# Performance work log

Measured on AMD Instinct MI355X. Metric: run time of the kernel, lower is better.

Reference implementation:

```python
import jax, jax.numpy as jnp
import numpy as np

RHO = 1.0
EPSILON = 0.1
N_ITERS = 5
EPS = 1e-08


def setup_inputs() -> dict:
    key = jax.random.key(0)
    k1, k2, k3 = jax.random.split(key, 3)
    B, H, M, N, D = 16, 16, 256, 576, 1024
    # student cross-attention weights: positive, rows roughly sum to 1 (post-softmax in the real model)
    sa = jax.random.uniform(k1, (B, H, M, N), dtype=jnp.float32) + 1e-3
    student_attn = sa / sa.sum(axis=-1, keepdims=True)
    visual_feats = jax.random.normal(k2, (B, N, D), dtype=jnp.float32)
    text_feats = jax.random.normal(k3, (B, M, D), dtype=jnp.float32)
    text_mask = jnp.ones((B, M), dtype=jnp.float32)
    return {"student_attn": student_attn, "visual_feats": visual_feats,
            "text_feats": text_feats, "text_mask": text_mask}


def _l2norm(x):
    return x / jnp.sqrt(jnp.sum(x * x, axis=-1, keepdims=True) + 1e-12)


def _teacher_plan(x, y, y_mask):
    # x: (B,N,D) visual, y: (B,M,D) text, y_mask: (B,M)
    B, N, D = x.shape
    M = y.shape[1]
    x_n = _l2norm(x)
    y_n = _l2norm(y)
    cost = 1.0 - jnp.einsum('bmd,bnd->bmn', y_n, x_n)          # (B,M,N)
    mu = jnp.full((B, N, 1), 1.0 / N, dtype=x.dtype)            # visual marginal (column vec)
    nu = (y_mask / (jnp.sum(y_mask, axis=1, keepdims=True) + EPS))[:, :, None]  # (B,M,1)
    K = jnp.exp(-cost / EPSILON)                                # (B,M,N)
    fi = RHO / (RHO + EPSILON)
    u = jnp.ones((B, M, 1), dtype=x.dtype)
    v = jnp.ones((B, N, 1), dtype=x.dtype)
    for _ in range(N_ITERS):
        Kv = jnp.einsum('bmn,bnk->bmk', K, v)                   # (B,M,1)
        u = (nu / (Kv + EPS)) ** fi
        Ktu = jnp.einsum('bmn,bmk->bnk', K, u)                  # (B,N,1)
        v = (mu / (Ktu + EPS)) ** fi
    P = u * K * jnp.swapaxes(v, 1, 2)                           # (B,M,N)
    return P / (jnp.sum(P, axis=-1, keepdims=True) + EPS)


def reference(student_attn, visual_feats, text_feats, text_mask):
    teacher = jax.lax.stop_gradient(_teacher_plan(visual_feats, text_feats, text_mask))
    teacher = teacher[:, None, :, :]                            # (B,1,M,N)
    loss = -jnp.sum(teacher * jnp.log(student_attn + EPS), axis=-1)  # (B,H,M)
    loss = loss * text_mask[:, None, :]
    return jnp.mean(loss)
```

## Files before the change

### kernel.cpp

```cpp
#include <hip/hip_runtime.h>
#include <math.h>

#define B_ 16
#define H_ 16
#define M_ 256
#define N_ 576
#define D_ 1024
#define BK 64
#define LDS_STRIDE (BK + 8)

constexpr float EPS_ = 1e-8f;
constexpr float FI_ = 0.90909090909090906f;

typedef __bf16 bf16x8 __attribute__((ext_vector_type(8)));
typedef float f32x4 __attribute__((ext_vector_type(4)));

__device__ __forceinline__ float wave_reduce(float v) {
#pragma unroll
  for (int o = 32; o > 0; o >>= 1) v += __shfl_down(v, o, 64);
  return v;
}

__device__ __forceinline__ unsigned short f2bf(float f) {
  union { float f; unsigned u; } a; a.f = f;
  unsigned r = a.u + 0x7fff + ((a.u >> 16) & 1);
  return (unsigned short)(r >> 16);
}

__global__ __launch_bounds__(256) void norm_bf16_kernel(const float* __restrict__ x,
                                                        unsigned short* __restrict__ out,
                                                        int rows) {
  int wave = (int)((blockIdx.x * blockDim.x + threadIdx.x) >> 6);
  int lane = threadIdx.x & 63;
  if (wave >= rows) return;
  const float* r = x + (size_t)wave * D_;
  float4 v[4];
  float s = 0.f;
#pragma unroll
  for (int it = 0; it < 4; ++it) {
    v[it] = *(const float4*)&r[it * 256 + lane * 4];
    s += v[it].x * v[it].x + v[it].y * v[it].y + v[it].z * v[it].z + v[it].w * v[it].w;
  }
  s = wave_reduce(s);
  s = __shfl(s, 0, 64);
  float inv = rsqrtf(s + 1e-12f);
  unsigned short* o = out + (size_t)wave * D_;
#pragma unroll
  for (int it = 0; it < 4; ++it) {
    ushort4 pk;
    pk.x = f2bf(v[it].x * inv);
    pk.y = f2bf(v[it].y * inv);
    pk.z = f2bf(v[it].z * inv);
    pk.w = f2bf(v[it].w * inv);
    *(ushort4*)&o[it * 256 + lane * 4] = pk;
  }
}

__global__ __launch_bounds__(256) void gemm_k_mfma(const unsigned short* __restrict__ xb,
                                                   const unsigned short* __restrict__ yb,
                                                   float* __restrict__ Kw) {
  __shared__ unsigned short As[64][LDS_STRIDE];
  __shared__ unsigned short Bs[64][LDS_STRIDE];
  const int b = blockIdx.z;
  const int m0 = blockIdx.y * 64;
  const int n0 = blockIdx.x * 64;
  const unsigned short* Y = yb + (size_t)b * M_ * D_;
  const unsigned short* X = xb + (size_t)b * N_ * D_;
  const int t = threadIdx.x;
  const int lane = t & 63;
  const int w = t >> 6;
  const int wm = (w & 1) * 32;
  const int wn = (w >> 1) * 32;
  const int lr = t >> 3;
  const int lc = (t & 7) * 8;
  const int fr = lane & 15;
  const int fk = (lane >> 4) * 8;

  f32x4 acc[2][2] = {};
  for (int k0 = 0; k0 < D_; k0 += BK) {
#pragma unroll
    for (int p = 0; p < 2; ++p) {
      *(uint4*)&As[lr + 32 * p][lc] = *(const uint4*)&Y[(size_t)(m0 + lr + 32 * p) * D_ + k0 + lc];
      *(uint4*)&Bs[lr + 32 * p][lc] = *(const uint4*)&X[(size_t)(n0 + lr + 32 * p) * D_ + k0 + lc];
    }
    __syncthreads();
#pragma unroll
    for (int ks = 0; ks < BK; ks += 32) {
      bf16x8 a[2], bfr[2];
#pragma unroll
      for (int i = 0; i < 2; ++i) {
        a[i] = *(const bf16x8*)&As[wm + i * 16 + fr][ks + fk];
        bfr[i] = *(const bf16x8*)&Bs[wn + i * 16 + fr][ks + fk];
      }
#pragma unroll
      for (int i = 0; i < 2; ++i)
#pragma unroll
        for (int j = 0; j < 2; ++j)
          acc[i][j] = __builtin_amdgcn_mfma_f32_16x16x32_bf16(a[i], bfr[j], acc[i][j], 0, 0, 0);
    }
    __syncthreads();
  }

  const int cm = (lane >> 4) * 4;
  const int cn = lane & 15;
#pragma unroll
  for (int i = 0; i < 2; ++i)
#pragma unroll
    for (int j = 0; j < 2; ++j)
#pragma unroll
      for (int rg = 0; rg < 4; ++rg) {
        int m = m0 + wm + i * 16 + cm + rg;
        int n = n0 + wn + j * 16 + cn;
        Kw[((size_t)b * M_ + m) * N_ + n] = expf(10.f * (acc[i][j][rg] - 1.f));
      }
}


__global__ __launch_bounds__(576) void sink_setup(const float* __restrict__ mask,
                                                  float* __restrict__ nu,
                                                  float* __restrict__ v) {
  __shared__ float sh_red[9];
  const int b = blockIdx.x;
  const int t = threadIdx.x;
  float mval = (t < M_) ? mask[b * M_ + t] : 0.f;
  float w = wave_reduce(mval);
  if ((t & 63) == 0) sh_red[t >> 6] = w;
  __syncthreads();
  float summ = 0.f;
#pragma unroll
  for (int i = 0; i < 9; ++i) summ += sh_red[i];
  if (t < M_) nu[b * M_ + t] = mval / (summ + EPS_);
  v[b * N_ + t] = 1.f;
}

__global__ __launch_bounds__(256) void sink_u(const float* __restrict__ Kw,
                                              const float* __restrict__ v,
                                              const float* __restrict__ nu,
                                              float* __restrict__ u) {
  const int b = blockIdx.y;
  const int row = blockIdx.x * 4 + (threadIdx.x >> 6);
  const int lane = threadIdx.x & 63;
  const float* rowp = Kw + ((size_t)b * M_ + row) * N_;
  const float* vb = v + b * N_;
  float s = 0.f;
#pragma unroll
  for (int k = 0; k < 9; ++k) s += rowp[lane + 64 * k] * vb[lane + 64 * k];
  s = wave_reduce(s);
  if (lane == 0) {
    int idx = b * M_ + row;
    u[idx] = powf(nu[idx] / (s + EPS_), FI_);
  }
}

__global__ __launch_bounds__(256) void sink_v(const float* __restrict__ Kw,
                                              const float* __restrict__ u,
                                              float* __restrict__ v) {
  __shared__ float part[4][64];
  const int b = blockIdx.y;
  const int n0 = blockIdx.x * 64;
  const int col = n0 + (threadIdx.x & 63);
  const int g = threadIdx.x >> 6;
  const float* Kb = Kw + (size_t)b * M_ * N_;
  const float* ub = u + b * M_;
  float s = 0.f;
#pragma unroll 8
  for (int m = g * 64; m < (g + 1) * 64; ++m) s += Kb[(size_t)m * N_ + col] * ub[m];
  part[g][threadIdx.x & 63] = s;
  __syncthreads();
  if (threadIdx.x < 64) {
    float tot = part[0][threadIdx.x] + part[1][threadIdx.x] +
                part[2][threadIdx.x] + part[3][threadIdx.x];
    v[b * N_ + n0 + threadIdx.x] = powf((1.f / (float)N_) / (tot + EPS_), FI_);
  }
}

__global__ __launch_bounds__(256) void sink_scale(const float* __restrict__ Kw,
                                                  const float* __restrict__ v,
                                                  const float* __restrict__ u,
                                                  const float* __restrict__ mask,
                                                  float* __restrict__ scale) {
  const int b = blockIdx.y;
  const int row = blockIdx.x * 4 + (threadIdx.x >> 6);
  const int lane = threadIdx.x & 63;
  const float* rowp = Kw + ((size_t)b * M_ + row) * N_;
  const float* vb = v + b * N_;
  float s = 0.f;
#pragma unroll
  for (int k = 0; k < 9; ++k) s += rowp[lane + 64 * k] * vb[lane + 64 * k];
  s = wave_reduce(s);
  if (lane == 0) {
    int idx = b * M_ + row;
    float uu = u[idx];
    scale[idx] = mask[idx] * uu / (uu * s + EPS_);
  }
}

__global__ __launch_bounds__(256) void loss_kernel(const float* __restrict__ student,
                                                   const float* __restrict__ Kw,
                                                   const float* __restrict__ v,
                                                   const float* __restrict__ scale,
                                                   float* __restrict__ out) {
  const unsigned TOT = (unsigned)B_ * H_ * M_ * (N_ / 4);
  __shared__ float sh[4];
  float acc = 0.f;
  for (unsigned idx = blockIdx.x * blockDim.x + threadIdx.x; idx < TOT;
       idx += gridDim.x * blockDim.x) {
    unsigned n4 = idx % (N_ / 4);
    unsigned rem = idx / (N_ / 4);
    unsigned m = rem & (M_ - 1);
    rem >>= 8;
    unsigned b = rem >> 4;
    float4 s4 = *(const float4*)&student[(size_t)idx * 4];
    float4 k4 = *(const float4*)&Kw[(size_t)(b * M_ + m) * N_ + n4 * 4];
    float4 v4 = *(const float4*)&v[(size_t)b * N_ + n4 * 4];
    float sc = scale[b * M_ + m];
    float tsum = k4.x * v4.x * __logf(s4.x + EPS_) + k4.y * v4.y * __logf(s4.y + EPS_) +
                 k4.z * v4.z * __logf(s4.z + EPS_) + k4.w * v4.w * __logf(s4.w + EPS_);
    acc -= sc * tsum;
  }
  float w = wave_reduce(acc);
  int lane = threadIdx.x & 63, wv = threadIdx.x >> 6;
  if (lane == 0) sh[wv] = w;
  __syncthreads();
  if (threadIdx.x == 0) {
    float tot = sh[0] + sh[1] + sh[2] + sh[3];
    atomicAdd(out, tot * (1.f / ((float)B_ * H_ * M_)));
  }
}

extern "C" void kernel_launch(void* const* d_in, const int* in_sizes, int n_in,
                              void* d_out, int out_size, void* d_ws, size_t ws_size,
                              hipStream_t stream) {
  const float* student = (const float*)d_in[0];
  const float* vis = (const float*)d_in[1];
  const float* txt = (const float*)d_in[2];
  const float* mask = (const float*)d_in[3];
  float* out = (float*)d_out;

  char* ws = (char*)d_ws;
  const size_t K_BYTES = (size_t)B_ * M_ * N_ * 4;
  float* Kw = (float*)ws;
  char* p = ws + K_BYTES;
  unsigned short* xb = (unsigned short*)p; p += (size_t)B_ * N_ * D_ * 2;
  unsigned short* ybf = (unsigned short*)p; p += (size_t)B_ * M_ * D_ * 2;
  float* vv = (float*)p;    p += B_ * N_ * 4;
  float* scale = (float*)p; p += B_ * M_ * 4;
  float* nu = (float*)p;    p += B_ * M_ * 4;
  float* uu = (float*)p;    p += B_ * M_ * 4;

  hipMemsetAsync(d_out, 0, sizeof(float), stream);
  norm_bf16_kernel<<<(B_ * N_) / 4, 256, 0, stream>>>(vis, xb, B_ * N_);
  norm_bf16_kernel<<<(B_ * M_) / 4, 256, 0, stream>>>(txt, ybf, B_ * M_);
  gemm_k_mfma<<<dim3(N_ / 64, M_ / 64, B_), 256, 0, stream>>>(xb, ybf, Kw);

  sink_setup<<<B_, N_, 0, stream>>>(mask, nu, vv);
  for (int it = 0; it < 5; ++it) {
    sink_u<<<dim3(M_ / 4, B_), 256, 0, stream>>>(Kw, vv, nu, uu);
    sink_v<<<dim3(N_ / 64, B_), 256, 0, stream>>>(Kw, uu, vv);
  }
  sink_scale<<<dim3(M_ / 4, B_), 256, 0, stream>>>(Kw, vv, uu, mask, scale);

  loss_kernel<<<4096, 256, 0, stream>>>(student, Kw, vv, scale, out);
}
```

Measured before the change: 349.0 us.

## Store K in bf16, merge prep kernels, fuse scale into per-row loss kernel

Merges the two normalization launches and the mask-sum setup into one prep kernel, and stores the exp cost matrix K as bf16 to halve its traffic across the Sinkhorn iterations. The first u-update skips the v read because v starts at one. The final scale pass is folded into a loss kernel with one block per (b,m) row, which caches K*v in LDS and reuses it across all heads. Storing K in bf16 adds rounding error to the plan, and the strided per-head student reads may coalesce less well than the old flat loop.

```diff
diff --git a/kernel.cpp b/kernel.cpp
--- a/kernel.cpp
+++ b/kernel.cpp
@@ -8,6 +8,7 @@
 #define D_ 1024
 #define BK 64
 #define LDS_STRIDE (BK + 8)
+#define NROWS (B_ * N_ + B_ * M_)
 
 constexpr float EPS_ = 1e-8f;
 constexpr float FI_ = 0.90909090909090906f;
@@ -27,38 +28,61 @@
   return (unsigned short)(r >> 16);
 }
 
-__global__ __launch_bounds__(256) void norm_bf16_kernel(const float* __restrict__ x,
-                                                        unsigned short* __restrict__ out,
-                                                        int rows) {
-  int wave = (int)((blockIdx.x * blockDim.x + threadIdx.x) >> 6);
-  int lane = threadIdx.x & 63;
-  if (wave >= rows) return;
-  const float* r = x + (size_t)wave * D_;
-  float4 v[4];
-  float s = 0.f;
-#pragma unroll
-  for (int it = 0; it < 4; ++it) {
-    v[it] = *(const float4*)&r[it * 256 + lane * 4];
-    s += v[it].x * v[it].x + v[it].y * v[it].y + v[it].z * v[it].z + v[it].w * v[it].w;
-  }
-  s = wave_reduce(s);
-  s = __shfl(s, 0, 64);
-  float inv = rsqrtf(s + 1e-12f);
-  unsigned short* o = out + (size_t)wave * D_;
-#pragma unroll
-  for (int it = 0; it < 4; ++it) {
-    ushort4 pk;
-    pk.x = f2bf(v[it].x * inv);
-    pk.y = f2bf(v[it].y * inv);
-    pk.z = f2bf(v[it].z * inv);
-    pk.w = f2bf(v[it].w * inv);
-    *(ushort4*)&o[it * 256 + lane * 4] = pk;
+__device__ __forceinline__ float bf2f(unsigned short u) {
+  union { unsigned u; float f; } a; a.u = ((unsigned)u) << 16;
+  return a.f;
+}
+
+__global__ __launch_bounds__(256) void prep_kernel(const float* __restrict__ vis,
+                                                   const float* __restrict__ txt,
+                                                   const float* __restrict__ mask,
+                                                   unsigned short* __restrict__ xb,
+                                                   unsigned short* __restrict__ yb,
+                                                   float* __restrict__ masksum) {
+  const int bid = blockIdx.x;
+  const int lane = threadIdx.x & 63;
+  if (bid < NROWS / 4) {
+    int wave = bid * 4 + (threadIdx.x >> 6);
+    const float* src;
+    unsigned short* dst;
+    if (wave < B_ * N_) {
+      src = vis + (size_t)wave * D_;
+      dst = xb + (size_t)wave * D_;
+    } else {
+      int r = wave - B_ * N_;
+      src = txt + (size_t)r * D_;
+      dst = yb + (size_t)r * D_;
+    }
+    float4 v[4];
+    float s = 0.f;
+#pragma unroll
+    for (int it = 0; it < 4; ++it) {
+      v[it] = *(const float4*)&src[it * 256 + lane * 4];
+      s += v[it].x * v[it].x + v[it].y * v[it].y + v[it].z * v[it].z + v[it].w * v[it].w;
+    }
+    s = wave_reduce(s);
+    s = __shfl(s, 0, 64);
+    float inv = rsqrtf(s + 1e-12f);
+#pragma unroll
+    for (int it = 0; it < 4; ++it) {
+      ushort4 pk;
+      pk.x = f2bf(v[it].x * inv);
+      pk.y = f2bf(v[it].y * inv);
+      pk.z = f2bf(v[it].z * inv);
+      pk.w = f2bf(v[it].w * inv);
+      *(ushort4*)&dst[it * 256 + lane * 4] = pk;
+    }
+  } else {
+    int b = (bid - NROWS / 4) * 4 + (threadIdx.x >> 6);
+    float4 mv = *(const float4*)&mask[b * M_ + lane * 4];
+    float s = wave_reduce(mv.x + mv.y + mv.z + mv.w);
+    if (lane == 0) masksum[b] = s;
   }
 }
 
 __global__ __launch_bounds__(256) void gemm_k_mfma(const unsigned short* __restrict__ xb,
                                                    const unsigned short* __restrict__ yb,
-                                                   float* __restrict__ Kw) {
+                                                   unsigned short* __restrict__ Kw) {
   __shared__ unsigned short As[64][LDS_STRIDE];
   __shared__ unsigned short Bs[64][LDS_STRIDE];
   const int b = blockIdx.z;
@@ -111,48 +135,52 @@
       for (int rg = 0; rg < 4; ++rg) {
         int m = m0 + wm + i * 16 + cm + rg;
         int n = n0 + wn + j * 16 + cn;
-        Kw[((size_t)b * M_ + m) * N_ + n] = expf(10.f * (acc[i][j][rg] - 1.f));
+        Kw[((size_t)b * M_ + m) * N_ + n] = f2bf(expf(10.f * (acc[i][j][rg] - 1.f)));
       }
 }
 
 
-__global__ __launch_bounds__(576) void sink_setup(const float* __restrict__ mask,
-                                                  float* __restrict__ nu,
-                                                  float* __restrict__ v) {
-  __shared__ float sh_red[9];
-  const int b = blockIdx.x;
-  const int t = threadIdx.x;
-  float mval = (t < M_) ? mask[b * M_ + t] : 0.f;
-  float w = wave_reduce(mval);
-  if ((t & 63) == 0) sh_red[t >> 6] = w;
-  __syncthreads();
-  float summ = 0.f;
-#pragma unroll
-  for (int i = 0; i < 9; ++i) summ += sh_red[i];
-  if (t < M_) nu[b * M_ + t] = mval / (summ + EPS_);
-  v[b * N_ + t] = 1.f;
-}
-
-__global__ __launch_bounds__(256) void sink_u(const float* __restrict__ Kw,
-                                              const float* __restrict__ v,
-                                              const float* __restrict__ nu,
-                                              float* __restrict__ u) {
+__global__ __launch_bounds__(256) void sink_u_first(const unsigned short* __restrict__ Kw,
+                                                    const float* __restrict__ mask,
+                                                    const float* __restrict__ masksum,
+                                                    float* __restrict__ u) {
   const int b = blockIdx.y;
   const int row = blockIdx.x * 4 + (threadIdx.x >> 6);
   const int lane = threadIdx.x & 63;
-  const float* rowp = Kw + ((size_t)b * M_ + row) * N_;
-  const float* vb = v + b * N_;
+  const unsigned short* rowp = Kw + ((size_t)b * M_ + row) * N_;
   float s = 0.f;
 #pragma unroll
-  for (int k = 0; k < 9; ++k) s += rowp[lane + 64 * k] * vb[lane + 64 * k];
+  for (int k = 0; k < 9; ++k) s += bf2f(rowp[lane + 64 * k]);
   s = wave_reduce(s);
   if (lane == 0) {
     int idx = b * M_ + row;
-    u[idx] = powf(nu[idx] / (s + EPS_), FI_);
-  }
-}
-
-__global__ __launch_bounds__(256) void sink_v(const float* __restrict__ Kw,
+    float nu = mask[idx] / (masksum[b] + EPS_);
+    u[idx] = powf(nu / (s + EPS_), FI_);
+  }
+}
+
+__global__ __launch_bounds__(256) void sink_u(const unsigned short* __restrict__ Kw,
+                                              const float* __restrict__ v,
+                                              const float* __restrict__ mask,
+                                              const float* __restrict__ masksum,
+                                              float* __restrict__ u) {
+  const int b = blockIdx.y;
+  const int row = blockIdx.x * 4 + (threadIdx.x >> 6);
+  const int lane = threadIdx.x & 63;
+  const unsigned short* rowp = Kw + ((size_t)b * M_ + row) * N_;
+  const float* vb = v + b * N_;
+  float s = 0.f;
+#pragma unroll
+  for (int k = 0; k < 9; ++k) s += bf2f(rowp[lane + 64 * k]) * vb[lane + 64 * k];
+  s = wave_reduce(s);
+  if (lane == 0) {
+    int idx = b * M_ + row;
+    float nu = mask[idx] / (masksum[b] + EPS_);
+    u[idx] = powf(nu / (s + EPS_), FI_);
+  }
+}
+
+__global__ __launch_bounds__(256) void sink_v(const unsigned short* __restrict__ Kw,
                                               const float* __restrict__ u,
                                               float* __restrict__ v) {
   __shared__ float part[4][64];
@@ -160,11 +188,11 @@
   const int n0 = blockIdx.x * 64;
   const int col = n0 + (threadIdx.x & 63);
   const int g = threadIdx.x >> 6;
-  const float* Kb = Kw + (size_t)b * M_ * N_;
+  const unsigned short* Kb = Kw + (size_t)b * M_ * N_;
   const float* ub = u + b * M_;
   float s = 0.f;
 #pragma unroll 8
-  for (int m = g * 64; m < (g + 1) * 64; ++m) s += Kb[(size_t)m * N_ + col] * ub[m];
+  for (int m = g * 64; m < (g + 1) * 64; ++m) s += bf2f(Kb[(size_t)m * N_ + col]) * ub[m];
   part[g][threadIdx.x & 63] = s;
   __syncthreads();
   if (threadIdx.x < 64) {
@@ -174,57 +202,52 @@
   }
 }
 
-__global__ __launch_bounds__(256) void sink_scale(const float* __restrict__ Kw,
+__global__ __launch_bounds__(256) void loss_fused(const float* __restrict__ student,
+                                                  const unsigned short* __restrict__ Kw,
                                                   const float* __restrict__ v,
-                                                  const float* __restrict__ u,
                                                   const float* __restrict__ mask,
-                                                  float* __restrict__ scale) {
-  const int b = blockIdx.y;
-  const int row = blockIdx.x * 4 + (threadIdx.x >> 6);
-  const int lane = threadIdx.x & 63;
-  const float* rowp = Kw + ((size_t)b * M_ + row) * N_;
+                                                  float* __restrict__ out) {
+  __shared__ float kv[N_];
+  __shared__ float red[4];
+  __shared__ float sh_scale;
+  const int m = blockIdx.x;
+  const int b = blockIdx.y;
+  const int t = threadIdx.x;
+
+  const unsigned short* rowp = Kw + ((size_t)b * M_ + m) * N_;
   const float* vb = v + b * N_;
-  float s = 0.f;
-#pragma unroll
-  for (int k = 0; k < 9; ++k) s += rowp[lane + 64 * k] * vb[lane + 64 * k];
-  s = wave_reduce(s);
-  if (lane == 0) {
-    int idx = b * M_ + row;
-    float uu = u[idx];
-    scale[idx] = mask[idx] * uu / (uu * s + EPS_);
-  }
-}
-
-__global__ __launch_bounds__(256) void loss_kernel(const float* __restrict__ student,
-                                                   const float* __restrict__ Kw,
-                                                   const float* __restrict__ v,
-                                                   const float* __restrict__ scale,
-                                                   float* __restrict__ out) {
-  const unsigned TOT = (unsigned)B_ * H_ * M_ * (N_ / 4);
-  __shared__ float sh[4];
+  float part = 0.f;
+  for (int i = t; i < N_; i += 256) {
+    float val = bf2f(rowp[i]) * vb[i];
+    kv[i] = val;
+    part += val;
+  }
+  part = wave_reduce(part);
+  if ((t & 63) == 0) red[t >> 6] = part;
+  __syncthreads();
+  if (t == 0) {
+    float Kv = red[0] + red[1] + red[2] + red[3];
+    sh_scale = mask[b * M_ + m] / (Kv + EPS_);
+  }
+
+  const float* st = student + ((size_t)b * H_ * M_ + m) * N_;
   float acc = 0.f;
-  for (unsigned idx = blockIdx.x * blockDim.x + threadIdx.x; idx < TOT;
-       idx += gridDim.x * blockDim.x) {
-    unsigned n4 = idx % (N_ / 4);
-    unsigned rem = idx / (N_ / 4);
-    unsigned m = rem & (M_ - 1);
-    rem >>= 8;
-    unsigned b = rem >> 4;
-    float4 s4 = *(const float4*)&student[(size_t)idx * 4];
-    float4 k4 = *(const float4*)&Kw[(size_t)(b * M_ + m) * N_ + n4 * 4];
-    float4 v4 = *(const float4*)&v[(size_t)b * N_ + n4 * 4];
-    float sc = scale[b * M_ + m];
-    float tsum = k4.x * v4.x * __logf(s4.x + EPS_) + k4.y * v4.y * __logf(s4.y + EPS_) +
-                 k4.z * v4.z * __logf(s4.z + EPS_) + k4.w * v4.w * __logf(s4.w + EPS_);
-    acc -= sc * tsum;
-  }
-  float w = wave_reduce(acc);
-  int lane = threadIdx.x & 63, wv = threadIdx.x >> 6;
-  if (lane == 0) sh[wv] = w;
-  __syncthreads();
-  if (threadIdx.x == 0) {
-    float tot = sh[0] + sh[1] + sh[2] + sh[3];
-    atomicAdd(out, tot * (1.f / ((float)B_ * H_ * M_)));
+#pragma unroll 1
+  for (int i = t; i < H_ * (N_ / 4); i += 256) {
+    int h = i / (N_ / 4);
+    int n4 = i - h * (N_ / 4);
+    float4 s4 = *(const float4*)&st[(size_t)h * M_ * N_ + n4 * 4];
+    float4 k4 = *(const float4*)&kv[n4 * 4];
+    acc -= k4.x * __logf(s4.x + EPS_) + k4.y * __logf(s4.y + EPS_) +
+           k4.z * __logf(s4.z + EPS_) + k4.w * __logf(s4.w + EPS_);
+  }
+  acc = wave_reduce(acc);
+  __syncthreads();
+  if ((t & 63) == 0) red[t >> 6] = acc;
+  __syncthreads();
+  if (t == 0) {
+    float tot = red[0] + red[1] + red[2] + red[3];
+    atomicAdd(out, sh_scale * tot * (1.f / ((float)B_ * H_ * M_)));
   }
 }
 
@@ -237,28 +260,24 @@
   const float* mask = (const float*)d_in[3];
   float* out = (float*)d_out;
 
-  char* ws = (char*)d_ws;
-  const size_t K_BYTES = (size_t)B_ * M_ * N_ * 4;
-  float* Kw = (float*)ws;
-  char* p = ws + K_BYTES;
+  char* p = (char*)d_ws;
+  unsigned short* Kb = (unsigned short*)p; p += (size_t)B_ * M_ * N_ * 2;
   unsigned short* xb = (unsigned short*)p; p += (size_t)B_ * N_ * D_ * 2;
-  unsigned short* ybf = (unsigned short*)p; p += (size_t)B_ * M_ * D_ * 2;
-  float* vv = (float*)p;    p += B_ * N_ * 4;
-  float* scale = (float*)p; p += B_ * M_ * 4;
-  float* nu = (float*)p;    p += B_ * M_ * 4;
-  float* uu = (float*)p;    p += B_ * M_ * 4;
+  unsigned short* yb = (unsigned short*)p; p += (size_t)B_ * M_ * D_ * 2;
+  float* vv = (float*)p;      p += B_ * N_ * 4;
+  float* uu = (float*)p;      p += B_ * M_ * 4;
+  float* msum = (float*)p;    p += B_ * 4;
 
   hipMemsetAsync(d_out, 0, sizeof(float), stream);
-  norm_bf16_kernel<<<(B_ * N_) / 4, 256, 0, stream>>>(vis, xb, B_ * N_);
-  norm_bf16_kernel<<<(B_ * M_) / 4, 256, 0, stream>>>(txt, ybf, B_ * M_);
-  gemm_k_mfma<<<dim3(N_ / 64, M_ / 64, B_), 256, 0, stream>>>(xb, ybf, Kw);
-
-  sink_setup<<<B_, N_, 0, stream>>>(mask, nu, vv);
-  for (int it = 0; it < 5; ++it) {
-    sink_u<<<dim3(M_ / 4, B_), 256, 0, stream>>>(Kw, vv, nu, uu);
-    sink_v<<<dim3(N_ / 64, B_), 256, 0, stream>>>(Kw, uu, vv);
-  }
-  sink_scale<<<dim3(M_ / 4, B_), 256, 0, stream>>>(Kw, vv, uu, mask, scale);
-
-  loss_kernel<<<4096, 256, 0, stream>>>(student, Kw, vv, scale, out);
-}
+  prep_kernel<<<NROWS / 4 + 4, 256, 0, stream>>>(vis, txt, mask, xb, yb, msum);
+  gemm_k_mfma<<<dim3(N_ / 64, M_ / 64, B_), 256, 0, stream>>>(xb, yb, Kb);
+
+  sink_u_first<<<dim3(M_ / 4, B_), 256, 0, stream>>>(Kb, mask, msum, uu);
+  sink_v<<<dim3(N_ / 64, B_), 256, 0, stream>>>(Kb, uu, vv);
+  for (int it = 1; it < 5; ++it) {
+    sink_u<<<dim3(M_ / 4, B_), 256, 0, stream>>>(Kb, vv, mask, msum, uu);
+    sink_v<<<dim3(N_ / 64, B_), 256, 0, stream>>>(Kb, uu, vv);
+  }
+
+  loss_fused<<<dim3(M_, B_), 256, 0, stream>>>(student, Kb, vv, mask, out);
+}
```

After: 353.0 us. No clear change (+1.2%).
